# Optimization experiments

Measured on AMD Instinct MI355X. Metric: run time of the kernel, lower is better.

Reference implementation:

```python
import jax, jax.numpy as jnp
import numpy as np
from functools import partial

B, T, C, HS = 8, 2048, 2048, 64
H = C // HS
LAYER_ID, N_LAYER, DIVISOR = 12, 24, 8.0


def setup_inputs() -> dict:
    key = jax.random.key(0)
    ks = jax.random.split(key, 6)
    x = jax.random.normal(ks[0], (B, T, C), jnp.float32)
    # faithful RWKV5 parameter initialization
    r01 = LAYER_ID / (N_LAYER - 1)
    r10 = 1.0 - LAYER_ID / N_LAYER
    ddd = np.arange(C, dtype=np.float64) / C
    tmk = (ddd ** r10).reshape(1, 1, C)
    tmv = tmk + 0.3 * r01
    tmr = (ddd ** (0.5 * r10)).reshape(1, 1, C)
    tmg = tmr.copy()
    n = np.arange(C, dtype=np.float64)
    decay = -6.0 + 5.0 * (n / (C - 1)) ** (0.7 + 1.3 * r01)
    zig = ((n + 1) % 3 - 1) * 0.1
    faaaa = r01 * (1.0 - n / (C - 1)) + zig
    f32 = lambda a: jnp.asarray(a, jnp.float32)
    W = lambda k: jax.random.normal(k, (C, C), jnp.float32) * 0.02
    return {
        'x': x,
        'time_mix_k': f32(tmk), 'time_mix_v': f32(tmv),
        'time_mix_r': f32(tmr), 'time_mix_g': f32(tmg),
        'time_decay': f32(decay.reshape(H, HS)),
        'time_faaaa': f32(faaaa.reshape(H, HS)),
        'Wr': W(ks[1]), 'Wk': W(ks[2]), 'Wv': W(ks[3]),
        'Wg': W(ks[4]), 'Wo': W(ks[5]),
        'ln_w': jnp.ones((C,), jnp.float32),
        'ln_b': jnp.zeros((C,), jnp.float32),
    }


def _wkv5(r, k, v, w, u):
    # r,k,v: [B,T,H,N]; w,u: [H,N]; sequential decayed linear attention
    rT = jnp.swapaxes(r, 0, 1)  # [T,B,H,N]
    kT = jnp.swapaxes(k, 0, 1)
    vT = jnp.swapaxes(v, 0, 1)
    wI = w[None, :, :, None]  # decay on key dim i of state S[b,h,i,j]
    uI = u[None, :, :, None]

    def step(S, rkv):
        r_t, k_t, v_t = rkv
        kv = jnp.einsum('bhi,bhj->bhij', k_t, v_t)
        y = jnp.einsum('bhi,bhij->bhj', r_t, S + uI * kv)
        return wI * S + kv, y

    S0 = jnp.zeros((r.shape[0], r.shape[2], r.shape[3], r.shape[3]), r.dtype)
    _, ys = jax.lax.scan(step, S0, (rT, kT, vT))
    return jnp.swapaxes(ys, 0, 1)  # [B,T,H,N]


def reference(x, time_mix_k, time_mix_v, time_mix_r, time_mix_g,
              time_decay, time_faaaa, Wr, Wk, Wv, Wg, Wo, ln_w, ln_b):
    # time shift: prepend zero row, drop last (ZeroPad2d((0,0,1,-1)))
    xx = jnp.pad(x, ((0, 0), (1, 0), (0, 0)))[:, :-1]
    xk = x * time_mix_k + xx * (1.0 - time_mix_k)
    xv = x * time_mix_v + xx * (1.0 - time_mix_v)
    xr = x * time_mix_r + xx * (1.0 - time_mix_r)
    xg = x * time_mix_g + xx * (1.0 - time_mix_g)
    r = (xr @ Wr).reshape(B, T, H, HS)
    k = (xk @ Wk).reshape(B, T, H, HS)
    v = (xv @ Wv).reshape(B, T, H, HS)
    g = jax.nn.silu(xg @ Wg)
    w = jnp.exp(-jnp.exp(time_decay))  # [H,N]
    y = _wkv5(r, k, v, w, time_faaaa)  # [B,T,H,N]
    # GroupNorm(H groups) over head_size, after /head_size_divisor
    yh = y / DIVISOR
    mu = jnp.mean(yh, axis=-1, keepdims=True)
    var = jnp.var(yh, axis=-1, keepdims=True)
    yn = (yh - mu) * jax.lax.rsqrt(var + 1e-5)
    yn = yn * ln_w.reshape(H, HS) + ln_b.reshape(H, HS)
    out = (yn.reshape(B, T, C) * g) @ Wo
    return out
```

## Files before the change

kernel.cpp:

```cpp
#include <hip/hip_runtime.h>
#include <hip/hip_bf16.h>

typedef __bf16 bf16_t;
typedef __bf16 bf16x8 __attribute__((ext_vector_type(8)));
typedef float f32x4 __attribute__((ext_vector_type(4)));

#define Bn 8
#define Tn 2048
#define Cn 2048
#define Hn 32
#define HSn 64
#define CT 64

static const long SZ = (long)Bn * Tn * Cn;

__device__ __forceinline__ void g2l16(const void* g, void* l) {
  __builtin_amdgcn_global_load_lds((const __attribute__((address_space(1))) void*)g,
                                   (__attribute__((address_space(3))) void*)l,
                                   16, 0, 0);
}

__global__ __launch_bounds__(256)
void transps(const float* w0, const float* w1, const float* w2,
             const float* w3, const float* w4, bf16_t* oh, bf16_t* ol)
{
  const float* Ws[5] = {w0, w1, w2, w3, w4};
  const float* W = Ws[blockIdx.z];
  const long base = (long)blockIdx.z * ((long)Cn * Cn);
  __shared__ float tile[64][65];
  const int xx = threadIdx.x & 63;
  const int y4 = threadIdx.x >> 6;
  const int bx = blockIdx.x * 64, by = blockIdx.y * 64;
#pragma unroll
  for (int i = 0; i < 16; ++i) {
    int row = i * 4 + y4;
    tile[row][xx] = W[(long)(by + row) * Cn + bx + xx];
  }
  __syncthreads();
#pragma unroll
  for (int i = 0; i < 16; ++i) {
    int row = i * 4 + y4;
    float v = tile[xx][row];
    bf16_t hi = (bf16_t)v;
    long o = base + (long)(bx + row) * Cn + by + xx;
    oh[o] = hi;
    ol[o] = (bf16_t)(v - (float)hi);
  }
}

__global__ __launch_bounds__(256)
void gemmx(const float* __restrict__ X, const float* __restrict__ tm,
           const bf16_t* __restrict__ Ah, const bf16_t* __restrict__ Al,
           const bf16_t* __restrict__ BTh, const bf16_t* __restrict__ BTl,
           void* __restrict__ Cp,
           const bf16_t* __restrict__ Zh, const bf16_t* __restrict__ Zl,
           bf16_t* __restrict__ Gh, bf16_t* __restrict__ Gl,
           int amode, int emode)
{
  __shared__ __align__(16) bf16_t lAh[128 * 32];
  __shared__ __align__(16) bf16_t lAl[128 * 32];
  __shared__ __align__(16) bf16_t lBh[128 * 32];
  __shared__ __align__(16) bf16_t lBl[128 * 32];

  const int tid = threadIdx.x;
  const int wave = tid >> 6;
  const int lane = tid & 63;
  const long m0 = (long)blockIdx.y * 128;
  const int n0 = blockIdx.x * 128;
  const int wm = (wave & 1) * 64;
  const int wn = (wave >> 1) * 64;

  const int e0 = (wave * 2 + 0) * 512 + lane * 8;
  const int e1 = (wave * 2 + 1) * 512 + lane * 8;
  const int r0 = e0 >> 5, s0 = (e0 & 31) >> 3;
  const int r1 = e1 >> 5, s1 = (e1 & 31) >> 3;
  const int c0 = (s0 ^ ((r0 >> 1) & 3)) << 3;
  const int c1 = (s1 ^ ((r1 >> 1) & 3)) << 3;
  const long aoff0 = (m0 + r0) * Cn + c0;
  const long aoff1 = (m0 + r1) * Cn + c1;
  const long boff0 = (long)(n0 + r0) * Cn + c0;
  const long boff1 = (long)(n0 + r1) * Cn + c1;
  const int t0 = (int)((m0 + r0) & (Tn - 1));
  const int t1 = (int)((m0 + r1) & (Tn - 1));

  f32x4 acc[4][4] = {};
  const int kg = lane >> 4;
  const int lr = lane & 15;
  const int kS = (kg ^ ((lr >> 1) & 3)) * 8;

  for (int k0 = 0; k0 < Cn; k0 += 32) {
    if (amode == 0) {
      float xf[16], pf[16], tf[16];
      *(f32x4*)&xf[0]  = *(const f32x4*)&X[aoff0 + k0];
      *(f32x4*)&xf[4]  = *(const f32x4*)&X[aoff0 + k0 + 4];
      *(f32x4*)&xf[8]  = *(const f32x4*)&X[aoff1 + k0];
      *(f32x4*)&xf[12] = *(const f32x4*)&X[aoff1 + k0 + 4];
      if (t0 > 0) {
        *(f32x4*)&pf[0] = *(const f32x4*)&X[aoff0 - Cn + k0];
        *(f32x4*)&pf[4] = *(const f32x4*)&X[aoff0 - Cn + k0 + 4];
      } else {
#pragma unroll
        for (int q = 0; q < 8; ++q) pf[q] = 0.f;
      }
      if (t1 > 0) {
        *(f32x4*)&pf[8]  = *(const f32x4*)&X[aoff1 - Cn + k0];
        *(f32x4*)&pf[12] = *(const f32x4*)&X[aoff1 - Cn + k0 + 4];
      } else {
#pragma unroll
        for (int q = 8; q < 16; ++q) pf[q] = 0.f;
      }
      *(f32x4*)&tf[0]  = *(const f32x4*)&tm[k0 + c0];
      *(f32x4*)&tf[4]  = *(const f32x4*)&tm[k0 + c0 + 4];
      *(f32x4*)&tf[8]  = *(const f32x4*)&tm[k0 + c1];
      *(f32x4*)&tf[12] = *(const f32x4*)&tm[k0 + c1 + 4];
      bf16x8 h0, l0, h1, l1;
#pragma unroll
      for (int q = 0; q < 8; ++q) {
        float o = pf[q] + tf[q] * (xf[q] - pf[q]);
        bf16_t hi = (bf16_t)o;
        h0[q] = hi; l0[q] = (bf16_t)(o - (float)hi);
      }
#pragma unroll
      for (int q = 0; q < 8; ++q) {
        float o = pf[8 + q] + tf[8 + q] * (xf[8 + q] - pf[8 + q]);
        bf16_t hi = (bf16_t)o;
        h1[q] = hi; l1[q] = (bf16_t)(o - (float)hi);
      }
      *(bf16x8*)&lAh[e0] = h0; *(bf16x8*)&lAl[e0] = l0;
      *(bf16x8*)&lAh[e1] = h1; *(bf16x8*)&lAl[e1] = l1;
    } else {
      g2l16(Ah + aoff0 + k0, &lAh[e0]);
      g2l16(Ah + aoff1 + k0, &lAh[e1]);
      g2l16(Al + aoff0 + k0, &lAl[e0]);
      g2l16(Al + aoff1 + k0, &lAl[e1]);
    }
    g2l16(BTh + boff0 + k0, &lBh[e0]);
    g2l16(BTh + boff1 + k0, &lBh[e1]);
    g2l16(BTl + boff0 + k0, &lBl[e0]);
    g2l16(BTl + boff1 + k0, &lBl[e1]);
    __syncthreads();
    bf16x8 ah[4], al[4], bh[4], bl[4];
#pragma unroll
    for (int t = 0; t < 4; ++t) {
      ah[t] = *(const bf16x8*)&lAh[(wm + t * 16 + lr) * 32 + kS];
      al[t] = *(const bf16x8*)&lAl[(wm + t * 16 + lr) * 32 + kS];
      bh[t] = *(const bf16x8*)&lBh[(wn + t * 16 + lr) * 32 + kS];
      bl[t] = *(const bf16x8*)&lBl[(wn + t * 16 + lr) * 32 + kS];
    }
#pragma unroll
    for (int i = 0; i < 4; ++i)
#pragma unroll
      for (int j = 0; j < 4; ++j) {
        acc[i][j] = __builtin_amdgcn_mfma_f32_16x16x32_bf16(al[i], bh[j], acc[i][j], 0, 0, 0);
        acc[i][j] = __builtin_amdgcn_mfma_f32_16x16x32_bf16(ah[i], bl[j], acc[i][j], 0, 0, 0);
        acc[i][j] = __builtin_amdgcn_mfma_f32_16x16x32_bf16(ah[i], bh[j], acc[i][j], 0, 0, 0);
      }
    __syncthreads();
  }

  const int qr = lane >> 4;
  const int cn = lane & 15;
#pragma unroll
  for (int i = 0; i < 4; ++i) {
#pragma unroll
    for (int j = 0; j < 4; ++j) {
#pragma unroll
      for (int rg = 0; rg < 4; ++rg) {
        long row = m0 + wm + i * 16 + qr * 4 + rg;
        int col = n0 + wn + j * 16 + cn;
        long off = row * Cn + col;
        float vv = acc[i][j][rg];
        if (emode == 0) {
          ((bf16_t*)Cp)[off] = (bf16_t)vv;
        } else if (emode == 1) {
          float z = (float)Zh[off] + (float)Zl[off];
          float zg = vv / (1.f + __expf(-vv)) * z;
          bf16_t hi = (bf16_t)zg;
          Gh[off] = hi;
          Gl[off] = (bf16_t)(zg - (float)hi);
        } else if (emode == 2) {
          ((float*)Cp)[off] = vv;
        } else {
          bf16_t hi = (bf16_t)vv;
          Gh[off] = hi;
          Gl[off] = (bf16_t)(vv - (float)hi);
        }
      }
    }
  }
}

__global__ __launch_bounds__(512)
void wkv5(const bf16_t* Rh, const bf16_t* __restrict__ Rl,
          const bf16_t* Km, const bf16_t* __restrict__ Vm,
          const float* __restrict__ decay, const float* __restrict__ faaaa,
          const float* __restrict__ lw, const float* __restrict__ lb,
          bf16_t* Zh, bf16_t* Zl)
{
  const int bh = blockIdx.x;
  const int b = bh >> 5;
  const int h = bh & 31;
  const int tid = threadIdx.x;
  const int j = tid >> 3;
  const int ic = tid & 7;
  const int i0 = ic * 8;

  float w[8], u[8], S[8];
#pragma unroll
  for (int q = 0; q < 8; ++q) {
    w[q] = expf(-expf(decay[h * 64 + i0 + q]));
    u[q] = faaaa[h * 64 + i0 + q];
    S[q] = 0.f;
  }

  __shared__ __align__(16) float sR[2][CT * 64];
  __shared__ __align__(16) float sK[2][CT * 64];
  __shared__ __align__(16) float sV[2][CT * 64];
  __shared__ __align__(16) float sY[CT * 64];
  __shared__ float sA[2][CT];

  const int e = tid * 8;
  const int tl = e >> 6;
  const int cc = e & 63;
  const long gbase = (long)b * Tn * Cn + h * 64 + cc;

  const int wv = tid >> 6;
  const int ln = tid & 63;
  const float lwv = lw[h * 64 + ln];
  const float lbv = lb[h * 64 + ln];

  bf16x8 prh, prl, pk, pv;
  auto issue = [&](int cch) {
    const long g = gbase + (long)(cch * CT + tl) * Cn;
    prh = *(const bf16x8*)&Rh[g];
    prl = *(const bf16x8*)&Rl[g];
    pk  = *(const bf16x8*)&Km[g];
    pv  = *(const bf16x8*)&Vm[g];
  };
  auto commit = [&](int bufA) {
    float apv = 0.f;
#pragma unroll
    for (int q = 0; q < 8; ++q) {
      float rf = (float)prh[q] + (float)prl[q];
      float kf = (float)pk[q];
      sR[bufA][e + q] = rf;
      sK[bufA][e + q] = kf;
      sV[bufA][e + q] = (float)pv[q];
      apv += (rf * u[q]) * kf;
    }
    apv += __shfl_xor(apv, 1);
    apv += __shfl_xor(apv, 2);
    apv += __shfl_xor(apv, 4);
    if (ic == 0) sA[bufA][tl] = apv;
  };

  issue(0); commit(0);
  __syncthreads();
  issue(1);

  const int NC = Tn / CT;
  for (int cch = 0; cch < NC; ++cch) {
    const int buf = cch & 1;
#pragma unroll 4
    for (int t = 0; t < CT; ++t) {
      float rr[8], kk[8];
      *(f32x4*)&rr[0] = *(const f32x4*)&sR[buf][t * 64 + i0];
      *(f32x4*)&rr[4] = *(const f32x4*)&sR[buf][t * 64 + i0 + 4];
      *(f32x4*)&kk[0] = *(const f32x4*)&sK[buf][t * 64 + i0];
      *(f32x4*)&kk[4] = *(const f32x4*)&sK[buf][t * 64 + i0 + 4];
      float vj = sV[buf][t * 64 + j];
      float yp = 0.f;
#pragma unroll
      for (int q = 0; q < 8; ++q) {
        yp += rr[q] * S[q];
        S[q] = w[q] * S[q] + kk[q] * vj;
      }
      yp += __shfl_xor(yp, 1);
      yp += __shfl_xor(yp, 2);
      yp += __shfl_xor(yp, 4);
      if (ic == 0) sY[t * 64 + j] = (yp + sA[buf][t] * vj) * 0.125f;
    }
    if (cch + 1 < NC) commit((cch + 1) & 1);
    __syncthreads();
    if (cch + 2 < NC) issue(cch + 2);

    const long zrow0 = ((long)b * Tn + (long)cch * CT) * Cn + h * 64 + ln;
#pragma unroll
    for (int q = 0; q < 8; ++q) {
      const int t = wv * 8 + q;
      float val = sY[t * 64 + ln];
      float s = val, s2 = val * val;
#pragma unroll
      for (int off = 1; off < 64; off <<= 1) {
        s  += __shfl_xor(s, off);
        s2 += __shfl_xor(s2, off);
      }
      float mu = s * (1.f / 64.f);
      float var = fmaxf(s2 * (1.f / 64.f) - mu * mu, 0.f);
      float rs = rsqrtf(var + 1e-5f);
      float zv = (val - mu) * rs * lwv + lbv;
      bf16_t zh = (bf16_t)zv;
      Zh[zrow0 + (long)t * Cn] = zh;
      Zl[zrow0 + (long)t * Cn] = (bf16_t)(zv - (float)zh);
    }
    __syncthreads();
  }
}

extern "C" void kernel_launch(void* const* d_in, const int* in_sizes, int n_in,
                              void* d_out, int out_size, void* d_ws, size_t ws_size,
                              hipStream_t stream)
{
  const float* x    = (const float*)d_in[0];
  const float* tmk  = (const float*)d_in[1];
  const float* tmv  = (const float*)d_in[2];
  const float* tmr  = (const float*)d_in[3];
  const float* tmg  = (const float*)d_in[4];
  const float* tdec = (const float*)d_in[5];
  const float* tfaa = (const float*)d_in[6];
  const float* Wr   = (const float*)d_in[7];
  const float* Wk   = (const float*)d_in[8];
  const float* Wv   = (const float*)d_in[9];
  const float* Wg   = (const float*)d_in[10];
  const float* Wo   = (const float*)d_in[11];
  const float* lnw  = (const float*)d_in[12];
  const float* lnb  = (const float*)d_in[13];

  char* ws = (char*)d_ws;
  const long WSZ = (long)Cn * Cn;
  const long SZB = SZ * 2;
  bf16_t* wTh = (bf16_t*)ws;
  bf16_t* wTl = (bf16_t*)(ws + 5 * WSZ * 2);
  bf16_t* sl0 = (bf16_t*)(ws + 10 * WSZ * 2);
  bf16_t* sl1 = (bf16_t*)(ws + 10 * WSZ * 2 + SZB);
  bf16_t* d0a = (bf16_t*)d_out;
  bf16_t* d0b = (bf16_t*)d_out + SZ;

  const dim3 gGrid(16, 128, 1);

  transps<<<dim3(32, 32, 5), 256, 0, stream>>>(Wr, Wk, Wv, Wg, Wo, wTh, wTl);

  gemmx<<<gGrid, 256, 0, stream>>>(x, tmr, nullptr, nullptr,
                                   wTh + 0 * WSZ, wTl + 0 * WSZ, nullptr,
                                   nullptr, nullptr, d0a, sl1, 0, 3);
  gemmx<<<gGrid, 256, 0, stream>>>(x, tmk, nullptr, nullptr,
                                   wTh + 1 * WSZ, wTl + 1 * WSZ, d0b,
                                   nullptr, nullptr, nullptr, nullptr, 0, 0);
  gemmx<<<gGrid, 256, 0, stream>>>(x, tmv, nullptr, nullptr,
                                   wTh + 2 * WSZ, wTl + 2 * WSZ, sl0,
                                   nullptr, nullptr, nullptr, nullptr, 0, 0);

  wkv5<<<256, 512, 0, stream>>>(d0a, sl1, d0b, sl0, tdec, tfaa, lnw, lnb,
                                d0a, d0b);

  gemmx<<<gGrid, 256, 0, stream>>>(x, tmg, nullptr, nullptr,
                                   wTh + 3 * WSZ, wTl + 3 * WSZ, nullptr,
                                   d0a, d0b, sl0, sl1, 0, 1);

  gemmx<<<gGrid, 256, 0, stream>>>(nullptr, nullptr, sl0, sl1,
                                   wTh + 4 * WSZ, wTl + 4 * WSZ, d_out,
                                   nullptr, nullptr, nullptr, nullptr, 1, 2);
}
```

Baseline: 3.506 ms.

## Rework split-bf16 GEMM into 256x256 double-buffered pipelined tiles

The GEMM kernel moves from 128x128 tiles with 256 threads to 256x256 tiles with 512 threads. Shared memory is now double-buffered, so global-to-LDS loads for the next K step overlap the MFMAs on the current one, using explicit waitcnt, barriers and setprio. The hi and lo halves are staged in two phases, and the mode branches become template parameters. The larger tile cuts global traffic per FLOP, at the cost of 128KB of LDS and higher register pressure, which may limit occupancy.

```diff
diff --git a/kernel.cpp b/kernel.cpp
--- a/kernel.cpp
+++ b/kernel.cpp
@@ -48,137 +48,188 @@
   }
 }
 
-__global__ __launch_bounds__(256)
+template <int AMODE, int EMODE>
+__global__ __launch_bounds__(512)
 void gemmx(const float* __restrict__ X, const float* __restrict__ tm,
            const bf16_t* __restrict__ Ah, const bf16_t* __restrict__ Al,
            const bf16_t* __restrict__ BTh, const bf16_t* __restrict__ BTl,
            void* __restrict__ Cp,
            const bf16_t* __restrict__ Zh, const bf16_t* __restrict__ Zl,
-           bf16_t* __restrict__ Gh, bf16_t* __restrict__ Gl,
-           int amode, int emode)
+           bf16_t* __restrict__ Gh, bf16_t* __restrict__ Gl)
 {
-  __shared__ __align__(16) bf16_t lAh[128 * 32];
-  __shared__ __align__(16) bf16_t lAl[128 * 32];
-  __shared__ __align__(16) bf16_t lBh[128 * 32];
-  __shared__ __align__(16) bf16_t lBl[128 * 32];
+  __shared__ __align__(16) bf16_t lAh[2][256 * 32];
+  __shared__ __align__(16) bf16_t lAl[2][256 * 32];
+  __shared__ __align__(16) bf16_t lBh[2][256 * 32];
+  __shared__ __align__(16) bf16_t lBl[2][256 * 32];
 
   const int tid = threadIdx.x;
-  const int wave = tid >> 6;
+  const int wv = tid >> 6;
   const int lane = tid & 63;
-  const long m0 = (long)blockIdx.y * 128;
-  const int n0 = blockIdx.x * 128;
-  const int wm = (wave & 1) * 64;
-  const int wn = (wave >> 1) * 64;
-
-  const int e0 = (wave * 2 + 0) * 512 + lane * 8;
-  const int e1 = (wave * 2 + 1) * 512 + lane * 8;
-  const int r0 = e0 >> 5, s0 = (e0 & 31) >> 3;
-  const int r1 = e1 >> 5, s1 = (e1 & 31) >> 3;
+  const int wmw = (wv >> 2) & 1;
+  const int wnw = wv & 3;
+  const long m0 = (long)blockIdx.y * 256;
+  const int n0 = blockIdx.x * 256;
+
+  const int e0 = tid * 8;
+  const int e1 = 4096 + tid * 8;
+  const int r0 = tid >> 2;
+  const int s0 = tid & 3;
   const int c0 = (s0 ^ ((r0 >> 1) & 3)) << 3;
-  const int c1 = (s1 ^ ((r1 >> 1) & 3)) << 3;
   const long aoff0 = (m0 + r0) * Cn + c0;
-  const long aoff1 = (m0 + r1) * Cn + c1;
+  const long aoff1 = (m0 + r0 + 128) * Cn + c0;
   const long boff0 = (long)(n0 + r0) * Cn + c0;
-  const long boff1 = (long)(n0 + r1) * Cn + c1;
-  const int t0 = (int)((m0 + r0) & (Tn - 1));
-  const int t1 = (int)((m0 + r1) & (Tn - 1));
-
-  f32x4 acc[4][4] = {};
+  const long boff1 = (long)(n0 + r0 + 128) * Cn + c0;
+  const bool p0ok = ((int)(m0 & (Tn - 1)) | r0) != 0;
+
   const int kg = lane >> 4;
   const int lr = lane & 15;
   const int kS = (kg ^ ((lr >> 1) & 3)) * 8;
 
-  for (int k0 = 0; k0 < Cn; k0 += 32) {
-    if (amode == 0) {
-      float xf[16], pf[16], tf[16];
-      *(f32x4*)&xf[0]  = *(const f32x4*)&X[aoff0 + k0];
-      *(f32x4*)&xf[4]  = *(const f32x4*)&X[aoff0 + k0 + 4];
-      *(f32x4*)&xf[8]  = *(const f32x4*)&X[aoff1 + k0];
-      *(f32x4*)&xf[12] = *(const f32x4*)&X[aoff1 + k0 + 4];
-      if (t0 > 0) {
-        *(f32x4*)&pf[0] = *(const f32x4*)&X[aoff0 - Cn + k0];
-        *(f32x4*)&pf[4] = *(const f32x4*)&X[aoff0 - Cn + k0 + 4];
-      } else {
-#pragma unroll
-        for (int q = 0; q < 8; ++q) pf[q] = 0.f;
-      }
-      if (t1 > 0) {
-        *(f32x4*)&pf[8]  = *(const f32x4*)&X[aoff1 - Cn + k0];
-        *(f32x4*)&pf[12] = *(const f32x4*)&X[aoff1 - Cn + k0 + 4];
-      } else {
-#pragma unroll
-        for (int q = 8; q < 16; ++q) pf[q] = 0.f;
-      }
-      *(f32x4*)&tf[0]  = *(const f32x4*)&tm[k0 + c0];
-      *(f32x4*)&tf[4]  = *(const f32x4*)&tm[k0 + c0 + 4];
-      *(f32x4*)&tf[8]  = *(const f32x4*)&tm[k0 + c1];
-      *(f32x4*)&tf[12] = *(const f32x4*)&tm[k0 + c1 + 4];
-      bf16x8 h0, l0, h1, l1;
-#pragma unroll
-      for (int q = 0; q < 8; ++q) {
-        float o = pf[q] + tf[q] * (xf[q] - pf[q]);
-        bf16_t hi = (bf16_t)o;
-        h0[q] = hi; l0[q] = (bf16_t)(o - (float)hi);
-      }
-#pragma unroll
-      for (int q = 0; q < 8; ++q) {
-        float o = pf[8 + q] + tf[8 + q] * (xf[8 + q] - pf[8 + q]);
-        bf16_t hi = (bf16_t)o;
-        h1[q] = hi; l1[q] = (bf16_t)(o - (float)hi);
-      }
-      *(bf16x8*)&lAh[e0] = h0; *(bf16x8*)&lAl[e0] = l0;
-      *(bf16x8*)&lAh[e1] = h1; *(bf16x8*)&lAl[e1] = l1;
+  auto mixA = [&](long kc2, int dst) {
+    float xf[16], pf[16], tf[8];
+    const long a0 = aoff0 + kc2, a1 = aoff1 + kc2;
+    *(f32x4*)&xf[0]  = *(const f32x4*)&X[a0];
+    *(f32x4*)&xf[4]  = *(const f32x4*)&X[a0 + 4];
+    *(f32x4*)&xf[8]  = *(const f32x4*)&X[a1];
+    *(f32x4*)&xf[12] = *(const f32x4*)&X[a1 + 4];
+    if (p0ok) {
+      *(f32x4*)&pf[0] = *(const f32x4*)&X[a0 - Cn];
+      *(f32x4*)&pf[4] = *(const f32x4*)&X[a0 - Cn + 4];
     } else {
-      g2l16(Ah + aoff0 + k0, &lAh[e0]);
-      g2l16(Ah + aoff1 + k0, &lAh[e1]);
-      g2l16(Al + aoff0 + k0, &lAl[e0]);
-      g2l16(Al + aoff1 + k0, &lAl[e1]);
-    }
-    g2l16(BTh + boff0 + k0, &lBh[e0]);
-    g2l16(BTh + boff1 + k0, &lBh[e1]);
-    g2l16(BTl + boff0 + k0, &lBl[e0]);
-    g2l16(BTl + boff1 + k0, &lBl[e1]);
-    __syncthreads();
-    bf16x8 ah[4], al[4], bh[4], bl[4];
-#pragma unroll
-    for (int t = 0; t < 4; ++t) {
-      ah[t] = *(const bf16x8*)&lAh[(wm + t * 16 + lr) * 32 + kS];
-      al[t] = *(const bf16x8*)&lAl[(wm + t * 16 + lr) * 32 + kS];
-      bh[t] = *(const bf16x8*)&lBh[(wn + t * 16 + lr) * 32 + kS];
-      bl[t] = *(const bf16x8*)&lBl[(wn + t * 16 + lr) * 32 + kS];
-    }
-#pragma unroll
-    for (int i = 0; i < 4; ++i)
-#pragma unroll
-      for (int j = 0; j < 4; ++j) {
+#pragma unroll
+      for (int q = 0; q < 8; ++q) pf[q] = 0.f;
+    }
+    *(f32x4*)&pf[8]  = *(const f32x4*)&X[a1 - Cn];
+    *(f32x4*)&pf[12] = *(const f32x4*)&X[a1 - Cn + 4];
+    *(f32x4*)&tf[0] = *(const f32x4*)&tm[kc2 + c0];
+    *(f32x4*)&tf[4] = *(const f32x4*)&tm[kc2 + c0 + 4];
+    bf16x8 h0, l0, h1, l1;
+#pragma unroll
+    for (int q = 0; q < 8; ++q) {
+      float o0 = pf[q] + tf[q] * (xf[q] - pf[q]);
+      bf16_t hi0 = (bf16_t)o0;
+      h0[q] = hi0; l0[q] = (bf16_t)(o0 - (float)hi0);
+      float o1 = pf[8 + q] + tf[q] * (xf[8 + q] - pf[8 + q]);
+      bf16_t hi1 = (bf16_t)o1;
+      h1[q] = hi1; l1[q] = (bf16_t)(o1 - (float)hi1);
+    }
+    *(bf16x8*)&lAh[dst][e0] = h0; *(bf16x8*)&lAl[dst][e0] = l0;
+    *(bf16x8*)&lAh[dst][e1] = h1; *(bf16x8*)&lAl[dst][e1] = l1;
+  };
+
+  if constexpr (AMODE == 0) {
+    mixA(0, 0);
+    g2l16(BTh + boff0, &lBh[0][e0]);
+    g2l16(BTh + boff1, &lBh[0][e1]);
+    __builtin_amdgcn_sched_barrier(0);
+    g2l16(BTl + boff0, &lBl[0][e0]);
+    g2l16(BTl + boff1, &lBl[0][e1]);
+  } else {
+    g2l16(Ah + aoff0, &lAh[0][e0]);
+    g2l16(Ah + aoff1, &lAh[0][e1]);
+    g2l16(BTh + boff0, &lBh[0][e0]);
+    g2l16(BTh + boff1, &lBh[0][e1]);
+    __builtin_amdgcn_sched_barrier(0);
+    g2l16(Al + aoff0, &lAl[0][e0]);
+    g2l16(Al + aoff1, &lAl[0][e1]);
+    g2l16(BTl + boff0, &lBl[0][e0]);
+    g2l16(BTl + boff1, &lBl[0][e1]);
+  }
+
+  const int NT = Cn / 32;
+  f32x4 acc[8][4] = {};
+  bf16x8 ah[8], bh[4];
+
+  for (int t = 0; t < NT; ++t) {
+    const int cb = t & 1, nb = cb ^ 1;
+    const int tn = (t + 1 < NT) ? t + 1 : 0;
+    const long kc = (long)tn * 32;
+
+    if constexpr (AMODE == 0) {
+      asm volatile("s_waitcnt vmcnt(2) lgkmcnt(0)" ::: "memory");
+    } else {
+      asm volatile("s_waitcnt vmcnt(4)" ::: "memory");
+    }
+    __builtin_amdgcn_sched_barrier(0);
+    __builtin_amdgcn_s_barrier();
+    __builtin_amdgcn_sched_barrier(0);
+    if constexpr (AMODE == 0) {
+      g2l16(BTh + boff0 + kc, &lBh[nb][e0]);
+      g2l16(BTh + boff1 + kc, &lBh[nb][e1]);
+      g2l16(BTl + boff0 + kc, &lBl[nb][e0]);
+      g2l16(BTl + boff1 + kc, &lBl[nb][e1]);
+    } else {
+      g2l16(Ah + aoff0 + kc, &lAh[nb][e0]);
+      g2l16(Ah + aoff1 + kc, &lAh[nb][e1]);
+      g2l16(BTh + boff0 + kc, &lBh[nb][e0]);
+      g2l16(BTh + boff1 + kc, &lBh[nb][e1]);
+    }
+#pragma unroll
+    for (int i = 0; i < 8; ++i)
+      ah[i] = *(const bf16x8*)&lAh[cb][(wmw * 128 + i * 16 + lr) * 32 + kS];
+#pragma unroll
+    for (int j = 0; j < 4; ++j)
+      bh[j] = *(const bf16x8*)&lBh[cb][(wnw * 64 + j * 16 + lr) * 32 + kS];
+    __builtin_amdgcn_s_setprio(1);
+#pragma unroll
+    for (int i = 0; i < 8; ++i)
+#pragma unroll
+      for (int j = 0; j < 4; ++j)
+        acc[i][j] = __builtin_amdgcn_mfma_f32_16x16x32_bf16(ah[i], bh[j], acc[i][j], 0, 0, 0);
+    __builtin_amdgcn_s_setprio(0);
+    if constexpr (AMODE == 0) mixA(kc, nb);
+
+    asm volatile("s_waitcnt vmcnt(4)" ::: "memory");
+    __builtin_amdgcn_sched_barrier(0);
+    __builtin_amdgcn_s_barrier();
+    __builtin_amdgcn_sched_barrier(0);
+    if constexpr (AMODE == 1) {
+      g2l16(Al + aoff0 + kc, &lAl[nb][e0]);
+      g2l16(Al + aoff1 + kc, &lAl[nb][e1]);
+      g2l16(BTl + boff0 + kc, &lBl[nb][e0]);
+      g2l16(BTl + boff1 + kc, &lBl[nb][e1]);
+    }
+    bf16x8 al[8], bl[4];
+#pragma unroll
+    for (int i = 0; i < 8; ++i)
+      al[i] = *(const bf16x8*)&lAl[cb][(wmw * 128 + i * 16 + lr) * 32 + kS];
+#pragma unroll
+    for (int j = 0; j < 4; ++j)
+      bl[j] = *(const bf16x8*)&lBl[cb][(wnw * 64 + j * 16 + lr) * 32 + kS];
+    __builtin_amdgcn_s_setprio(1);
+#pragma unroll
+    for (int i = 0; i < 8; ++i) {
+#pragma unroll
+      for (int j = 0; j < 4; ++j)
         acc[i][j] = __builtin_amdgcn_mfma_f32_16x16x32_bf16(al[i], bh[j], acc[i][j], 0, 0, 0);
+#pragma unroll
+      for (int j = 0; j < 4; ++j)
         acc[i][j] = __builtin_amdgcn_mfma_f32_16x16x32_bf16(ah[i], bl[j], acc[i][j], 0, 0, 0);
-        acc[i][j] = __builtin_amdgcn_mfma_f32_16x16x32_bf16(ah[i], bh[j], acc[i][j], 0, 0, 0);
-      }
-    __syncthreads();
+    }
+    __builtin_amdgcn_s_setprio(0);
   }
 
   const int qr = lane >> 4;
-  const int cn = lane & 15;
-#pragma unroll
-  for (int i = 0; i < 4; ++i) {
+  const int cnn = lane & 15;
+#pragma unroll
+  for (int i = 0; i < 8; ++i) {
 #pragma unroll
     for (int j = 0; j < 4; ++j) {
 #pragma unroll
       for (int rg = 0; rg < 4; ++rg) {
-        long row = m0 + wm + i * 16 + qr * 4 + rg;
-        int col = n0 + wn + j * 16 + cn;
+        long row = m0 + wmw * 128 + i * 16 + qr * 4 + rg;
+        int col = n0 + wnw * 64 + j * 16 + cnn;
         long off = row * Cn + col;
         float vv = acc[i][j][rg];
-        if (emode == 0) {
+        if constexpr (EMODE == 0) {
           ((bf16_t*)Cp)[off] = (bf16_t)vv;
-        } else if (emode == 1) {
+        } else if constexpr (EMODE == 1) {
           float z = (float)Zh[off] + (float)Zl[off];
           float zg = vv / (1.f + __expf(-vv)) * z;
           bf16_t hi = (bf16_t)zg;
           Gh[off] = hi;
           Gl[off] = (bf16_t)(zg - (float)hi);
-        } else if (emode == 2) {
+        } else if constexpr (EMODE == 2) {
           ((float*)Cp)[off] = vv;
         } else {
           bf16_t hi = (bf16_t)vv;
@@ -336,28 +387,28 @@
   bf16_t* d0a = (bf16_t*)d_out;
   bf16_t* d0b = (bf16_t*)d_out + SZ;
 
-  const dim3 gGrid(16, 128, 1);
+  const dim3 gGrid(8, 64, 1);
 
   transps<<<dim3(32, 32, 5), 256, 0, stream>>>(Wr, Wk, Wv, Wg, Wo, wTh, wTl);
 
-  gemmx<<<gGrid, 256, 0, stream>>>(x, tmr, nullptr, nullptr,
-                                   wTh + 0 * WSZ, wTl + 0 * WSZ, nullptr,
-                                   nullptr, nullptr, d0a, sl1, 0, 3);
-  gemmx<<<gGrid, 256, 0, stream>>>(x, tmk, nullptr, nullptr,
-                                   wTh + 1 * WSZ, wTl + 1 * WSZ, d0b,
-                                   nullptr, nullptr, nullptr, nullptr, 0, 0);
-  gemmx<<<gGrid, 256, 0, stream>>>(x, tmv, nullptr, nullptr,
-                                   wTh + 2 * WSZ, wTl + 2 * WSZ, sl0,
-                                   nullptr, nullptr, nullptr, nullptr, 0, 0);
+  gemmx<0, 3><<<gGrid, 512, 0, stream>>>(x, tmr, nullptr, nullptr,
+                                         wTh + 0 * WSZ, wTl + 0 * WSZ, nullptr,
+                                         nullptr, nullptr, d0a, sl1);
+  gemmx<0, 0><<<gGrid, 512, 0, stream>>>(x, tmk, nullptr, nullptr,
+                                         wTh + 1 * WSZ, wTl + 1 * WSZ, d0b,
+                                         nullptr, nullptr, nullptr, nullptr);
+  gemmx<0, 0><<<gGrid, 512, 0, stream>>>(x, tmv, nullptr, nullptr,
+                                         wTh + 2 * WSZ, wTl + 2 * WSZ, sl0,
+                                         nullptr, nullptr, nullptr, nullptr);
 
   wkv5<<<256, 512, 0, stream>>>(d0a, sl1, d0b, sl0, tdec, tfaa, lnw, lnb,
                                 d0a, d0b);
 
-  gemmx<<<gGrid, 256, 0, stream>>>(x, tmg, nullptr, nullptr,
-                                   wTh + 3 * WSZ, wTl + 3 * WSZ, nullptr,
-                                   d0a, d0b, sl0, sl1, 0, 1);
-
-  gemmx<<<gGrid, 256, 0, stream>>>(nullptr, nullptr, sl0, sl1,
-                                   wTh + 4 * WSZ, wTl + 4 * WSZ, d_out,
-                                   nullptr, nullptr, nullptr, nullptr, 1, 2);
+  gemmx<0, 1><<<gGrid, 512, 0, stream>>>(x, tmg, nullptr, nullptr,
+                                         wTh + 3 * WSZ, wTl + 3 * WSZ, nullptr,
+                                         d0a, d0b, sl0, sl1);
+
+  gemmx<1, 2><<<gGrid, 512, 0, stream>>>(nullptr, nullptr, sl0, sl1,
+                                         wTh + 4 * WSZ, wTl + 4 * WSZ, d_out,
+                                         nullptr, nullptr, nullptr, nullptr);
 }
```

Measured after the change: 3.031 ms. 1.16x faster.
